# Kernel optimization log

Hardware: AMD Instinct MI355X
Metric: run time of the kernel (lower is better)

The kernel has to match this reference:

```python
import jax, jax.numpy as jnp
import numpy as np

N_NAT, N_UNNAT, N_OPSIN, N_CLUSTER, N_ELEC = 128, 128, 4, 64, 32
T = 65536
D_OPSIN = N_OPSIN * N_CLUSTER  # 256


def setup_inputs() -> dict:
    key = jax.random.key(0)
    ks = jax.random.split(key, 16)
    s = 0.01
    return {
        "x_nat_0": jax.random.normal(ks[0], (N_NAT,), jnp.float32),
        "x_unnat_0": jax.random.normal(ks[1], (N_UNNAT,), jnp.float32),
        "x_opsin_0": jax.random.normal(ks[2], (D_OPSIN,), jnp.float32),
        "U": jax.random.normal(ks[3], (T, N_ELEC), jnp.float32),
        # learnable params (0.01*randn as in __init__)
        "A_natnat": s * jax.random.normal(ks[4], (N_NAT, N_NAT), jnp.float32),
        "K_nat": s * jax.random.normal(ks[5], (N_NAT, 1), jnp.float32),
        "C_y_nat": s * jax.random.normal(ks[6], (1, N_NAT), jnp.float32),
        "A_unnatunnat": s * jax.random.normal(ks[7], (N_UNNAT, N_UNNAT), jnp.float32),
        "K_unnat": s * jax.random.normal(ks[8], (N_UNNAT, 1), jnp.float32),
        "C_y_unnat": s * jax.random.normal(ks[9], (1, N_UNNAT), jnp.float32),
        "Bp_nat": s * jax.random.normal(ks[10], (N_NAT, N_CLUSTER), jnp.float32),
        "Bp_unnat": s * jax.random.normal(ks[11], (N_UNNAT, N_CLUSTER), jnp.float32),
        # linear OpsinModel sub-system (source not provided; see notes)
        "A_opsin": s * jax.random.normal(ks[12], (D_OPSIN, D_OPSIN), jnp.float32),
        "B_opsin": s * jax.random.normal(ks[13], (D_OPSIN, N_ELEC), jnp.float32),
        "C_opsin": s * jax.random.normal(ks[14], (N_CLUSTER, D_OPSIN), jnp.float32),
    }


def _simulate(x_nat_0, x_unnat_0, x_opsin_0, U,
              A_natnat, K_nat, C_y_nat, A_unnatunnat, K_unnat, C_y_unnat,
              Bp_nat, Bp_unnat, A_opsin, B_opsin, C_opsin):
    k_nat = K_nat[:, 0]      # (N_nat,)
    k_unnat = K_unnat[:, 0]  # (N_unnat,)

    def step(carry, u_t):
        x_nat, x_unnat, x_opsin = carry
        # y[t] = C_y_nat x_nat + C_y_unnat x_unnat  -> shape (1,)
        y = C_y_nat @ x_nat + C_y_unnat @ x_unnat
        # photocurrents computed from CURRENT x_opsin (pre-update), as in torch code
        ph = C_opsin @ x_opsin  # (N_cluster,)
        c_yx = C_y_nat @ x_nat  # (1,)
        x_nat_n = A_natnat @ x_nat + k_nat * y + Bp_nat @ ph
        x_unnat_n = (A_unnatunnat @ x_unnat - k_unnat * c_yx
                     + k_unnat * y + Bp_unnat @ ph)
        x_opsin_n = A_opsin @ x_opsin + B_opsin @ u_t
        return (x_nat_n, x_unnat_n, x_opsin_n), (y[0], x_nat_n, x_unnat_n, x_opsin_n)

    init = (x_nat_0, x_unnat_0, x_opsin_0)
    _, (y_preds, nat_h, unnat_h, opsin_h) = jax.lax.scan(step, init, U)
    x_nat_hist = jnp.concatenate([x_nat_0[None], nat_h], axis=0)      # (T+1, N_nat)
    x_unnat_hist = jnp.concatenate([x_unnat_0[None], unnat_h], axis=0)
    x_opsin_hist = jnp.concatenate([x_opsin_0[None], opsin_h], axis=0)
    return y_preds, x_nat_hist, x_unnat_hist, x_opsin_hist


def reference(x_nat_0, x_unnat_0, x_opsin_0, U,
              A_natnat, K_nat, C_y_nat, A_unnatunnat, K_unnat, C_y_unnat,
              Bp_nat, Bp_unnat, A_opsin, B_opsin, C_opsin):
    return _simulate(x_nat_0, x_unnat_0, x_opsin_0, U,
                     A_natnat, K_nat, C_y_nat, A_unnatunnat, K_unnat, C_y_unnat,
                     Bp_nat, Bp_unnat, A_opsin, B_opsin, C_opsin)
```

## Files before the change

kernel.cpp:

```cpp
#include <hip/hip_runtime.h>

#define T_STEPS 65536
#define D_TAPS  8
#define NZ      512
#define KTOT    (D_TAPS * 32)
#define BT      32
#define NBLK    256
#define MTILES  ((T_STEPS + 1 + BT - 1) / BT)

typedef __attribute__((ext_vector_type(8))) short  short8;
typedef __attribute__((ext_vector_type(4))) short  short4v;
typedef __attribute__((ext_vector_type(4))) float  floatx4;

__device__ float g_M[NZ * NZ];
__device__ float g_Zeta[D_TAPS * NZ];
__device__ float g_BH[2][33 * NZ];
__device__ short g_Gbf[NZ * KTOT];

__device__ __forceinline__ short f2bf(float v) {
    unsigned int b = __float_as_uint(v);
    unsigned int r = (b + 0x7FFFu + ((b >> 16) & 1u)) >> 16;
    return (short)r;
}

__global__ __launch_bounds__(256) void k_build(
    const float* __restrict__ xn0, const float* __restrict__ xu0, const float* __restrict__ xo0,
    const float* __restrict__ Ann, const float* __restrict__ Kn,  const float* __restrict__ Cn,
    const float* __restrict__ Auu, const float* __restrict__ Ku,  const float* __restrict__ Cu,
    const float* __restrict__ Bpn, const float* __restrict__ Bpu,
    const float* __restrict__ Ao,  const float* __restrict__ Bo,  const float* __restrict__ Co,
    float* __restrict__ out)
{
    int q = blockIdx.x * 256 + threadIdx.x;
    int i = q >> 9, j = q & 511;
    float v;
    if (i < 128) {
        if (j < 128)       v = Ann[i * 128 + j] + Kn[i] * Cn[j];
        else if (j < 256)  v = Kn[i] * Cu[j - 128];
        else {
            int jp = j - 256; float s = 0.f;
            #pragma unroll 8
            for (int c = 0; c < 64; c++) s += Bpn[i * 64 + c] * Co[c * 256 + jp];
            v = s;
        }
    } else if (i < 256) {
        int ip = i - 128;
        if (j < 128)       v = 0.f;
        else if (j < 256)  { int jp = j - 128; v = Auu[ip * 128 + jp] + Ku[ip] * Cu[jp]; }
        else {
            int jp = j - 256; float s = 0.f;
            #pragma unroll 8
            for (int c = 0; c < 64; c++) s += Bpu[ip * 64 + c] * Co[c * 256 + jp];
            v = s;
        }
    } else {
        int ip = i - 256;
        v = (j >= 256) ? Ao[ip * 256 + (j - 256)] : 0.f;
    }
    g_M[q] = v;

    if (q < T_STEPS) out[q] = 0.f;

    if (q < 33 * NZ) {
        int jj = q & 511, cc = q >> 9;
        if (cc < 32) {
            float b = (jj >= 256) ? Bo[(jj - 256) * 32 + cc] : 0.f;
            g_BH[0][cc * NZ + jj]   = b;
            g_Gbf[jj * KTOT + cc]   = f2bf(b);
        } else {
            float z0j = (jj < 128) ? xn0[jj] : (jj < 256 ? xu0[jj - 128] : xo0[jj - 256]);
            g_BH[0][32 * NZ + jj] = z0j;
            g_Zeta[jj]            = z0j;
        }
    }
}

__global__ __launch_bounds__(256) void k_chain(int d)
{
    int q  = blockIdx.x * 256 + threadIdx.x;
    int o  = q >> 3;
    int sl = q & 7;
    int i  = o & 511, c = o >> 9;
    const float4* Mrow = (const float4*)(g_M + (size_t)i * NZ);
    const float4* srow = (const float4*)(g_BH[d & 1] + (size_t)c * NZ);
    float s = 0.f;
    #pragma unroll
    for (int k = 0; k < 16; k++) {
        float4 m = Mrow[k * 8 + sl], x = srow[k * 8 + sl];
        s += m.x * x.x + m.y * x.y + m.z * x.z + m.w * x.w;
    }
    s += __shfl_xor(s, 1, 64);
    s += __shfl_xor(s, 2, 64);
    s += __shfl_xor(s, 4, 64);
    if (sl == 0) {
        g_BH[(d & 1) ^ 1][c * NZ + i] = s;
        if (c < 32) g_Gbf[(size_t)i * KTOT + (d + 1) * 32 + c] = f2bf(s);
        else        g_Zeta[(d + 1) * NZ + i] = s;
    }
}

__global__ __launch_bounds__(512) void k_fir(
    const float* __restrict__ U, const float* __restrict__ Cn, const float* __restrict__ Cu,
    float* __restrict__ out)
{
    const int tid  = threadIdx.x;
    const int w    = tid >> 6;
    const int lane = tid & 63;
    const int quad = lane >> 4;
    const int lq   = lane & 15;
    const int col0 = w * 64;

    __shared__ short u_wv[2][8][40 * 40];

    short8 bfr[D_TAPS][4];
    #pragma unroll
    for (int kt = 0; kt < D_TAPS; kt++)
        #pragma unroll
        for (int nt = 0; nt < 4; nt++)
            bfr[kt][nt] = *(const short8*)(g_Gbf +
                (size_t)(col0 + nt * 16 + lq) * KTOT + kt * 32 + quad * 8);

    float cyv[4];
    #pragma unroll
    for (int nt = 0; nt < 4; nt++) {
        int i = col0 + nt * 16 + lq;
        cyv[nt] = (w < 2) ? Cn[i] : (w < 4 ? Cu[i - 128] : 0.f);
    }

    const size_t O1 = (size_t)T_STEPS;
    const size_t O2 = O1 + (size_t)(T_STEPS + 1) * 128;
    const size_t O3 = O2 + (size_t)(T_STEPS + 1) * 128;
    float* obase; int ostr, cbase;
    if      (w < 2) { obase = out + O1; ostr = 128; cbase = col0; }
    else if (w < 4) { obase = out + O2; ostr = 128; cbase = col0 - 128; }
    else            { obase = out + O3; ostr = 256; cbase = col0 - 256; }

    float4 st[5];
    {
        const int t0_ = blockIdx.x * BT;
        #pragma unroll
        for (int i = 0; i < 5; i++) {
            int fidx = i * 64 + lane, row = fidx >> 3, c4 = fidx & 7;
            int gr = t0_ - D_TAPS + row;
            st[i] = (gr >= 0 && gr < T_STEPS)
                  ? *(const float4*)(U + (size_t)gr * 32 + c4 * 4)
                  : make_float4(0.f, 0.f, 0.f, 0.f);
        }
    }

    int buf = 0;
    #pragma unroll 1
    for (int tb = blockIdx.x; tb < MTILES; tb += NBLK) {
        const int t0 = tb * BT;

        #pragma unroll
        for (int i = 0; i < 5; i++) {
            int fidx = i * 64 + lane, row = fidx >> 3, c4 = fidx & 7;
            short4v b;
            b.x = f2bf(st[i].x); b.y = f2bf(st[i].y);
            b.z = f2bf(st[i].z); b.w = f2bf(st[i].w);
            *(short4v*)&u_wv[buf][w][row * 40 + c4 * 4] = b;
        }

        const int nb = tb + NBLK;
        if (nb < MTILES) {
            const int t0n = nb * BT;
            #pragma unroll
            for (int i = 0; i < 5; i++) {
                int fidx = i * 64 + lane, row = fidx >> 3, c4 = fidx & 7;
                int gr = t0n - D_TAPS + row;
                st[i] = (gr >= 0 && gr < T_STEPS)
                      ? *(const float4*)(U + (size_t)gr * 32 + c4 * 4)
                      : make_float4(0.f, 0.f, 0.f, 0.f);
            }
        }

        floatx4 acc[2][4];
        #pragma unroll
        for (int mt = 0; mt < 2; mt++)
            #pragma unroll
            for (int nt = 0; nt < 4; nt++)
                acc[mt][nt] = (floatx4){0.f, 0.f, 0.f, 0.f};

        const short* ub = u_wv[buf][w];
        #pragma unroll
        for (int kt = 0; kt < D_TAPS; kt++) {
            short8 a[2];
            #pragma unroll
            for (int mt = 0; mt < 2; mt++) {
                const int r = mt * 16 + lq + (D_TAPS - 1) - kt;
                a[mt] = *(const short8*)&ub[r * 40 + quad * 8];
            }
            #pragma unroll
            for (int nt = 0; nt < 4; nt++)
                #pragma unroll
                for (int mt = 0; mt < 2; mt++)
                    acc[mt][nt] = __builtin_amdgcn_mfma_f32_16x16x32_bf16(
                                      a[mt], bfr[kt][nt], acc[mt][nt], 0, 0, 0);
        }

        #pragma unroll
        for (int mt = 0; mt < 2; mt++) {
            #pragma unroll
            for (int r = 0; r < 4; r++) {
                const int lrow = mt * 16 + quad * 4 + r;
                const int gt = t0 + lrow;
                const bool valid = (gt <= T_STEPS);
                float p = 0.f;
                #pragma unroll
                for (int nt = 0; nt < 4; nt++) {
                    float v = acc[mt][nt][r];
                    if (gt < D_TAPS) v += g_Zeta[gt * NZ + col0 + nt * 16 + lq];
                    if (valid)
                        obase[(size_t)gt * ostr + cbase + nt * 16 + lq] = v;
                    p = fmaf(cyv[nt], v, p);
                }
                if (w < 4) {
                    p += __shfl_xor(p, 1, 64);
                    p += __shfl_xor(p, 2, 64);
                    p += __shfl_xor(p, 4, 64);
                    p += __shfl_xor(p, 8, 64);
                    if (lq == 0 && gt < T_STEPS) atomicAdd(out + gt, p);
                }
            }
        }

        buf ^= 1;
    }
}

extern "C" void kernel_launch(void* const* d_in, const int* in_sizes, int n_in,
                              void* d_out, int out_size, void* d_ws, size_t ws_size,
                              hipStream_t stream)
{
    const float* xn0 = (const float*)d_in[0];
    const float* xu0 = (const float*)d_in[1];
    const float* xo0 = (const float*)d_in[2];
    const float* U   = (const float*)d_in[3];
    const float* Ann = (const float*)d_in[4];
    const float* Kn  = (const float*)d_in[5];
    const float* Cn  = (const float*)d_in[6];
    const float* Auu = (const float*)d_in[7];
    const float* Ku  = (const float*)d_in[8];
    const float* Cu  = (const float*)d_in[9];
    const float* Bpn = (const float*)d_in[10];
    const float* Bpu = (const float*)d_in[11];
    const float* Ao  = (const float*)d_in[12];
    const float* Bo  = (const float*)d_in[13];
    const float* Co  = (const float*)d_in[14];
    float* out = (float*)d_out;

    k_build<<<dim3(1024), dim3(256), 0, stream>>>(xn0, xu0, xo0, Ann, Kn, Cn,
                                                  Auu, Ku, Cu, Bpn, Bpu, Ao, Bo, Co, out);
    for (int d = 0; d < D_TAPS - 1; d++)
        k_chain<<<dim3(528), dim3(256), 0, stream>>>(d);

    k_fir<<<dim3(NBLK), dim3(512), 0, stream>>>(U, Cn, Cu, out);
}
```

Measured before the change: 236.2 us.

## Fuse build, chain and FIR kernels into one cooperative kernel with grid syncs

Merges the matrix build kernel, the seven chain-power kernels and the FIR kernel into a single cooperative launch, separating the stages with grid-wide barriers. The aim is to remove about eight kernel launch overheads and inter-kernel gaps. The chain work is redistributed so the 256x512 grid covers the 32 B-columns while the first 4096 threads also handle the state column. The cost is grid.sync overhead, and the FIR phase now runs with the register pressure of the fused kernel, which could lower occupancy.

```diff
diff --git a/kernel.cpp b/kernel.cpp
--- a/kernel.cpp
+++ b/kernel.cpp
@@ -1,4 +1,7 @@
 #include <hip/hip_runtime.h>
+#include <hip/hip_cooperative_groups.h>
+
+namespace cg = cooperative_groups;
 
 #define T_STEPS 65536
 #define D_TAPS  8
@@ -6,6 +9,8 @@
 #define KTOT    (D_TAPS * 32)
 #define BT      32
 #define NBLK    256
+#define NTHR    512
+#define GTHREADS (NBLK * NTHR)
 #define MTILES  ((T_STEPS + 1 + BT - 1) / BT)
 
 typedef __attribute__((ext_vector_type(8))) short  short8;
@@ -23,46 +28,54 @@
     return (short)r;
 }
 
-__global__ __launch_bounds__(256) void k_build(
+__global__ __launch_bounds__(512) void k_fused(
     const float* __restrict__ xn0, const float* __restrict__ xu0, const float* __restrict__ xo0,
+    const float* __restrict__ U,
     const float* __restrict__ Ann, const float* __restrict__ Kn,  const float* __restrict__ Cn,
     const float* __restrict__ Auu, const float* __restrict__ Ku,  const float* __restrict__ Cu,
     const float* __restrict__ Bpn, const float* __restrict__ Bpu,
     const float* __restrict__ Ao,  const float* __restrict__ Bo,  const float* __restrict__ Co,
     float* __restrict__ out)
 {
-    int q = blockIdx.x * 256 + threadIdx.x;
-    int i = q >> 9, j = q & 511;
-    float v;
-    if (i < 128) {
-        if (j < 128)       v = Ann[i * 128 + j] + Kn[i] * Cn[j];
-        else if (j < 256)  v = Kn[i] * Cu[j - 128];
-        else {
-            int jp = j - 256; float s = 0.f;
-            #pragma unroll 8
-            for (int c = 0; c < 64; c++) s += Bpn[i * 64 + c] * Co[c * 256 + jp];
-            v = s;
-        }
-    } else if (i < 256) {
-        int ip = i - 128;
-        if (j < 128)       v = 0.f;
-        else if (j < 256)  { int jp = j - 128; v = Auu[ip * 128 + jp] + Ku[ip] * Cu[jp]; }
-        else {
-            int jp = j - 256; float s = 0.f;
-            #pragma unroll 8
-            for (int c = 0; c < 64; c++) s += Bpu[ip * 64 + c] * Co[c * 256 + jp];
-            v = s;
-        }
-    } else {
-        int ip = i - 256;
-        v = (j >= 256) ? Ao[ip * 256 + (j - 256)] : 0.f;
-    }
-    g_M[q] = v;
-
-    if (q < T_STEPS) out[q] = 0.f;
-
-    if (q < 33 * NZ) {
-        int jj = q & 511, cc = q >> 9;
+    cg::grid_group grid = cg::this_grid();
+    const int tid  = threadIdx.x;
+    const int gtid = blockIdx.x * NTHR + tid;
+
+    #pragma unroll
+    for (int rep = 0; rep < 2; rep++) {
+        int q = gtid + rep * GTHREADS;
+        int i = q >> 9, j = q & 511;
+        float v;
+        if (i < 128) {
+            if (j < 128)       v = Ann[i * 128 + j] + Kn[i] * Cn[j];
+            else if (j < 256)  v = Kn[i] * Cu[j - 128];
+            else {
+                int jp = j - 256; float s = 0.f;
+                #pragma unroll 8
+                for (int c = 0; c < 64; c++) s += Bpn[i * 64 + c] * Co[c * 256 + jp];
+                v = s;
+            }
+        } else if (i < 256) {
+            int ip = i - 128;
+            if (j < 128)       v = 0.f;
+            else if (j < 256)  { int jp = j - 128; v = Auu[ip * 128 + jp] + Ku[ip] * Cu[jp]; }
+            else {
+                int jp = j - 256; float s = 0.f;
+                #pragma unroll 8
+                for (int c = 0; c < 64; c++) s += Bpu[ip * 64 + c] * Co[c * 256 + jp];
+                v = s;
+            }
+        } else {
+            int ip = i - 256;
+            v = (j >= 256) ? Ao[ip * 256 + (j - 256)] : 0.f;
+        }
+        g_M[q] = v;
+    }
+
+    if (gtid < T_STEPS) out[gtid] = 0.f;
+
+    if (gtid < 33 * NZ) {
+        int jj = gtid & 511, cc = gtid >> 9;
         if (cc < 32) {
             float b = (jj >= 256) ? Bo[(jj - 256) * 32 + cc] : 0.f;
             g_BH[0][cc * NZ + jj]   = b;
@@ -73,37 +86,54 @@
             g_Zeta[jj]            = z0j;
         }
     }
-}
-
-__global__ __launch_bounds__(256) void k_chain(int d)
-{
-    int q  = blockIdx.x * 256 + threadIdx.x;
-    int o  = q >> 3;
-    int sl = q & 7;
-    int i  = o & 511, c = o >> 9;
-    const float4* Mrow = (const float4*)(g_M + (size_t)i * NZ);
-    const float4* srow = (const float4*)(g_BH[d & 1] + (size_t)c * NZ);
-    float s = 0.f;
-    #pragma unroll
-    for (int k = 0; k < 16; k++) {
-        float4 m = Mrow[k * 8 + sl], x = srow[k * 8 + sl];
-        s += m.x * x.x + m.y * x.y + m.z * x.z + m.w * x.w;
-    }
-    s += __shfl_xor(s, 1, 64);
-    s += __shfl_xor(s, 2, 64);
-    s += __shfl_xor(s, 4, 64);
-    if (sl == 0) {
-        g_BH[(d & 1) ^ 1][c * NZ + i] = s;
-        if (c < 32) g_Gbf[(size_t)i * KTOT + (d + 1) * 32 + c] = f2bf(s);
-        else        g_Zeta[(d + 1) * NZ + i] = s;
-    }
-}
-
-__global__ __launch_bounds__(512) void k_fir(
-    const float* __restrict__ U, const float* __restrict__ Cn, const float* __restrict__ Cu,
-    float* __restrict__ out)
-{
-    const int tid  = threadIdx.x;
+
+    grid.sync();
+
+    #pragma unroll 1
+    for (int d = 0; d < D_TAPS - 1; d++) {
+        const float* __restrict__ src = g_BH[d & 1];
+        float*       __restrict__ dst = g_BH[(d & 1) ^ 1];
+        {
+            int o  = gtid >> 3;
+            int sl = gtid & 7;
+            int i  = o & 511, c = o >> 9;
+            const float4* Mrow = (const float4*)(g_M + (size_t)i * NZ);
+            const float4* srow = (const float4*)(src + (size_t)c * NZ);
+            float s = 0.f;
+            #pragma unroll
+            for (int k = 0; k < 16; k++) {
+                float4 m = Mrow[k * 8 + sl], x = srow[k * 8 + sl];
+                s += m.x * x.x + m.y * x.y + m.z * x.z + m.w * x.w;
+            }
+            s += __shfl_xor(s, 1, 64);
+            s += __shfl_xor(s, 2, 64);
+            s += __shfl_xor(s, 4, 64);
+            if (sl == 0) {
+                dst[c * NZ + i] = s;
+                g_Gbf[(size_t)i * KTOT + (d + 1) * 32 + c] = f2bf(s);
+            }
+        }
+        if (gtid < 4096) {
+            int sl = gtid & 7, i = gtid >> 3;
+            const float4* Mrow = (const float4*)(g_M + (size_t)i * NZ);
+            const float4* srow = (const float4*)(src + 32 * NZ);
+            float s = 0.f;
+            #pragma unroll
+            for (int k = 0; k < 16; k++) {
+                float4 m = Mrow[k * 8 + sl], x = srow[k * 8 + sl];
+                s += m.x * x.x + m.y * x.y + m.z * x.z + m.w * x.w;
+            }
+            s += __shfl_xor(s, 1, 64);
+            s += __shfl_xor(s, 2, 64);
+            s += __shfl_xor(s, 4, 64);
+            if (sl == 0) {
+                dst[32 * NZ + i]      = s;
+                g_Zeta[(d + 1) * NZ + i] = s;
+            }
+        }
+        grid.sync();
+    }
+
     const int w    = tid >> 6;
     const int lane = tid & 63;
     const int quad = lane >> 4;
@@ -250,10 +280,14 @@
     const float* Co  = (const float*)d_in[14];
     float* out = (float*)d_out;
 
-    k_build<<<dim3(1024), dim3(256), 0, stream>>>(xn0, xu0, xo0, Ann, Kn, Cn,
-                                                  Auu, Ku, Cu, Bpn, Bpu, Ao, Bo, Co, out);
-    for (int d = 0; d < D_TAPS - 1; d++)
-        k_chain<<<dim3(528), dim3(256), 0, stream>>>(d);
-
-    k_fir<<<dim3(NBLK), dim3(512), 0, stream>>>(U, Cn, Cu, out);
+    void* kargs[] = {
+        (void*)&xn0, (void*)&xu0, (void*)&xo0, (void*)&U,
+        (void*)&Ann, (void*)&Kn,  (void*)&Cn,
+        (void*)&Auu, (void*)&Ku,  (void*)&Cu,
+        (void*)&Bpn, (void*)&Bpu,
+        (void*)&Ao,  (void*)&Bo,  (void*)&Co,
+        (void*)&out
+    };
+    hipLaunchCooperativeKernel(reinterpret_cast<const void*>(k_fused),
+                               dim3(NBLK), dim3(NTHR), kargs, 0, stream);
 }
```

New measurement: 466.4 us. +97.4%, slower.
